# Performance work log

Measured on AMD Instinct MI355X. Metric: run time of the kernel, lower is better.

The kernel has to match this reference:

```python
import jax, jax.numpy as jnp
import numpy as np

DIM = 192
HEADS = 8
B, H, W = 8, 128, 128

def _dwconv3x3(x, w):
    # x: [B,C,H,W], w: [C,1,3,3] depthwise
    return jax.lax.conv_general_dilated(
        x, w, window_strides=(1, 1), padding=((1, 1), (1, 1)),
        dimension_numbers=('NCHW', 'OIHW', 'NCHW'),
        feature_group_count=x.shape[1])

def _proj(x, pw, dw):
    # 1x1 pointwise (as einsum) followed by 3x3 depthwise
    y = jnp.einsum('bchw,oc->bohw', x, pw)
    return _dwconv3x3(y, dw)

def setup_inputs() -> dict:
    key = jax.random.key(0)
    ks = jax.random.split(key, 9)
    s_pw = 1.0 / np.sqrt(DIM)
    s_dw = 1.0 / 3.0
    return {
        'x_feat': jax.random.normal(ks[0], (B, DIM, H, W), jnp.float32),
        'y_feat': jax.random.normal(ks[1], (B, DIM, H, W), jnp.float32),
        'q_pw': jax.random.normal(ks[2], (DIM, DIM), jnp.float32) * s_pw,
        'q_dw': jax.random.normal(ks[3], (DIM, 1, 3, 3), jnp.float32) * s_dw,
        'k_pw': jax.random.normal(ks[4], (DIM, DIM), jnp.float32) * s_pw,
        'k_dw': jax.random.normal(ks[5], (DIM, 1, 3, 3), jnp.float32) * s_dw,
        'v_pw': jax.random.normal(ks[6], (DIM, DIM), jnp.float32) * s_pw,
        'v_dw': jax.random.normal(ks[7], (DIM, 1, 3, 3), jnp.float32) * s_dw,
        'proj_w': jax.random.normal(ks[8], (DIM, DIM), jnp.float32) * s_pw,
        'temperature': jnp.ones((HEADS, 1, 1), jnp.float32),
    }

def reference(x_feat, y_feat, q_pw, q_dw, k_pw, k_dw, v_pw, v_dw, proj_w, temperature):
    b, c, h, w = x_feat.shape
    ch = c // HEADS  # channels per head
    q = _proj(x_feat, q_pw, q_dw)
    k = _proj(y_feat, k_pw, k_dw)
    v = _proj(y_feat, v_pw, v_dw)
    # b (head c) h w -> b head c (h w)
    to_heads = lambda t: t.reshape(b, HEADS, ch, h * w)
    q, k, v = to_heads(q), to_heads(k), to_heads(v)
    # L2-normalize along token dim (torch F.normalize eps=1e-12)
    q = q / jnp.maximum(jnp.linalg.norm(q, axis=-1, keepdims=True), 1e-12)
    k = k / jnp.maximum(jnp.linalg.norm(k, axis=-1, keepdims=True), 1e-12)
    attn = jnp.einsum('bhcn,bhdn->bhcd', q, k) * temperature  # [b,heads,ch,ch]
    attn = jax.nn.softmax(attn, axis=-1)
    out = jnp.einsum('bhcd,bhdn->bhcn', attn, v)
    out = out.reshape(b, c, h, w)
    out = jnp.einsum('bchw,oc->bohw', out, proj_w)
    return out
```

## Files before the change

kernel.cpp:

```cpp
#include <hip/hip_runtime.h>
#include <hip/hip_bf16.h>

#define BATCH 8
#define CDIM 192
#define HEADS 8
#define CH 24
#define HH 128
#define WW 128
#define NPIX (HH*WW)
#define NELEM (BATCH*CDIM*NPIX)
#define NP4 (NPIX/4)

#define DSLAB 16
#define NJOBS 624

typedef __attribute__((ext_vector_type(8))) short bf16x8;
typedef __attribute__((ext_vector_type(4))) float f32x4;
typedef __attribute__((ext_vector_type(4))) unsigned int u32x4;
typedef __attribute__((ext_vector_type(4))) unsigned short u16x4;

#define UNIT 100663296ull
__device__ __align__(256) unsigned char g_pool[4 * UNIT + (16u << 20)];

#define OFF_T0   (0 * UNIT)
#define OFF_QB   (1 * UNIT)
#define OFF_KB   (2 * UNIT)
#define OFF_V    (3 * UNIT)
#define OFF_MISC (4 * UNIT)
#define OFF_PART (OFF_MISC)
#define OFF_S    (OFF_MISC + 2555904ull)
#define OFF_M    (OFF_S + 159744ull)
#define OFF_MF   (OFF_M + 1179648ull)

__device__ inline unsigned short bf_rne(float x) {
  unsigned u = __float_as_uint(x);
  unsigned r = (u + 0x7fffu + ((u >> 16) & 1u)) >> 16;
  return (unsigned short)r;
}
__device__ inline void f32_split(float x, unsigned short& h, unsigned short& l) {
  h = bf_rne(x);
  float hf = __uint_as_float(((unsigned)h) << 16);
  l = bf_rne(x - hf);
}

__global__ __launch_bounds__(64) void w_to_frag(const float* __restrict__ W,
                                                unsigned short* __restrict__ F,
                                                int nb) {
  const int b = blockIdx.x / 12, mf = blockIdx.x % 12;
  const int lane = threadIdx.x;
  const int row = mf * 16 + (lane & 15);
  const size_t lo = (size_t)nb * CDIM * CDIM;
#pragma unroll
  for (int ks = 0; ks < 6; ++ks) {
    const int k0 = ks * 32 + (lane >> 4) * 8;
    const float* src = W + ((size_t)b * CDIM + row) * CDIM + k0;
    bf16x8 hv, lv;
#pragma unroll
    for (int j = 0; j < 8; ++j) {
      unsigned short h, l;
      f32_split(src[j], h, l);
      hv[j] = (short)h;
      lv[j] = (short)l;
    }
    const size_t didx = (((size_t)(blockIdx.x) * 6 + ks) * 64 + lane) * 8;
    *(bf16x8*)(F + didx) = hv;
    *(bf16x8*)(F + lo + didx) = lv;
  }
}

__global__ __launch_bounds__(256, 2) void mfma_gemm192(
    const float* __restrict__ X,
    const unsigned short* __restrict__ WF, size_t w_lo,
    int w_bstride,
    float* __restrict__ Out) {
  const int bn = blockIdx.x;
  const int b = blockIdx.y;
  const int t = threadIdx.x;
  const int lane = t & 63, wid = t >> 6;
  const int wm = wid >> 1, wn = wid & 1;
  const int kq = lane >> 4;

  __shared__ float Xs[32][132];

  const size_t wbase = (size_t)b * w_bstride;
  const float* Xb = X + (size_t)b * CDIM * NPIX;
  const int col4 = (t & 31) * 4;
  const int r0 = t >> 5;
  const int pxl = wn * 64 + (lane & 15);

  f32x4 acc[6][4];
#pragma unroll
  for (int mi = 0; mi < 6; ++mi)
#pragma unroll
    for (int ni = 0; ni < 4; ++ni) acc[mi][ni] = (f32x4){0.f, 0.f, 0.f, 0.f};

  for (int ks = 0; ks < 6; ++ks) {
    float4 st[4];
#pragma unroll
    for (int p = 0; p < 4; ++p)
      st[p] = *(const float4*)(Xb + (size_t)(ks * 32 + r0 + 8 * p) * NPIX +
                               bn * 128 + col4);
#pragma unroll
    for (int p = 0; p < 4; ++p)
      *(float4*)&Xs[r0 + 8 * p][col4 ^ ((p & 1) << 4)] = st[p];
    __syncthreads();

    bf16x8 Ah[6], Al[6];
#pragma unroll
    for (int mi = 0; mi < 6; ++mi) {
      const int mf = wm * 6 + mi;
      const size_t idx = wbase + (((size_t)(mf * 6 + ks)) * 64 + lane) * 8;
      Ah[mi] = *(const bf16x8*)(WF + idx);
      Al[mi] = *(const bf16x8*)(WF + w_lo + idx);
    }

    u32x4 Bh[4], Bl[4];
#pragma unroll
    for (int ni = 0; ni < 4; ++ni) {
      const int pxs = (pxl + ni * 16) ^ ((kq & 1) << 4);
#pragma unroll
      for (int jp = 0; jp < 4; ++jp) {
        const float x0 = Xs[kq * 8 + 2 * jp][pxs];
        const float x1 = Xs[kq * 8 + 2 * jp + 1][pxs];
        const unsigned u0 = __float_as_uint(x0);
        const unsigned u1 = __float_as_uint(x1);
        Bh[ni][jp] = (u1 & 0xffff0000u) | (u0 >> 16);
        const float rr0 = x0 - __uint_as_float(u0 & 0xffff0000u);
        const float rr1 = x1 - __uint_as_float(u1 & 0xffff0000u);
        Bl[ni][jp] = ((unsigned)bf_rne(rr1) << 16) | (unsigned)bf_rne(rr0);
      }
    }
    __syncthreads();

#pragma unroll
    for (int mi = 0; mi < 6; ++mi)
#pragma unroll
      for (int ni = 0; ni < 4; ++ni) {
        const bf16x8 bh = __builtin_bit_cast(bf16x8, Bh[ni]);
        const bf16x8 bl = __builtin_bit_cast(bf16x8, Bl[ni]);
        acc[mi][ni] = __builtin_amdgcn_mfma_f32_16x16x32_bf16(
            Ah[mi], bh, acc[mi][ni], 0, 0, 0);
        acc[mi][ni] = __builtin_amdgcn_mfma_f32_16x16x32_bf16(
            Ah[mi], bl, acc[mi][ni], 0, 0, 0);
        acc[mi][ni] = __builtin_amdgcn_mfma_f32_16x16x32_bf16(
            Al[mi], bh, acc[mi][ni], 0, 0, 0);
      }
  }

  const int ocol = bn * 128 + wn * 64 + (lane & 15);
  const int orow = wm * 96 + (lane >> 4) * 4;
#pragma unroll
  for (int mi = 0; mi < 6; ++mi)
#pragma unroll
    for (int r = 0; r < 4; ++r) {
      const int och = orow + mi * 16 + r;
      float* dst = Out + ((size_t)b * CDIM + och) * NPIX + ocol;
#pragma unroll
      for (int ni = 0; ni < 4; ++ni) dst[ni * 16] = acc[mi][ni][r];
    }
}

__global__ __launch_bounds__(256) void dwconv(const float* __restrict__ In,
                                              const float* __restrict__ Wd,
                                              float* __restrict__ Out) {
  const int idx = blockIdx.x * 256 + threadIdx.x;
  if (idx >= NELEM / 4) return;
  const int x4 = (idx & 31) * 4;
  const int y = (idx >> 5) & 127;
  const int c = (idx >> 12) % CDIM;
  const int b = idx / (32 * 128 * CDIM);

  const float* base = In + (size_t)(b * CDIM + c) * NPIX;
  float w[9];
#pragma unroll
  for (int i = 0; i < 9; ++i) w[i] = Wd[c * 9 + i];

  float acc0 = 0.f, acc1 = 0.f, acc2 = 0.f, acc3 = 0.f;
#pragma unroll
  for (int dy = 0; dy < 3; ++dy) {
    const int yy = y + dy - 1;
    if (yy < 0 || yy > 127) continue;
    const float* row = base + yy * WW;
    float vb0 = (x4 > 0) ? row[x4 - 1] : 0.f;
    const float4 m = *(const float4*)(row + x4);
    const float vb5 = (x4 + 4 < WW) ? row[x4 + 4] : 0.f;
    const float w0 = w[dy * 3 + 0], w1 = w[dy * 3 + 1], w2 = w[dy * 3 + 2];
    acc0 += w0 * vb0 + w1 * m.x + w2 * m.y;
    acc1 += w0 * m.x + w1 * m.y + w2 * m.z;
    acc2 += w0 * m.y + w1 * m.z + w2 * m.w;
    acc3 += w0 * m.z + w1 * m.w + w2 * vb5;
  }
  float4 o;
  o.x = acc0; o.y = acc1; o.z = acc2; o.w = acc3;
  *(float4*)(Out + (size_t)idx * 4) = o;
}

__global__ __launch_bounds__(256) void dwconv_bf(const float* __restrict__ In,
                                                 const float* __restrict__ Wd,
                                                 unsigned short* __restrict__ Out) {
  const int idx = blockIdx.x * 256 + threadIdx.x;
  if (idx >= NELEM / 4) return;
  const int x4 = (idx & 31) * 4;
  const int y = (idx >> 5) & 127;
  const int c = (idx >> 12) % CDIM;
  const int b = idx / (32 * 128 * CDIM);

  const float* base = In + (size_t)(b * CDIM + c) * NPIX;
  float w[9];
#pragma unroll
  for (int i = 0; i < 9; ++i) w[i] = Wd[c * 9 + i];

  float a[4] = {0.f, 0.f, 0.f, 0.f};
#pragma unroll
  for (int dy = 0; dy < 3; ++dy) {
    const int yy = y + dy - 1;
    if (yy < 0 || yy > 127) continue;
    const float* row = base + yy * WW;
    float vb0 = (x4 > 0) ? row[x4 - 1] : 0.f;
    const float4 m = *(const float4*)(row + x4);
    const float vb5 = (x4 + 4 < WW) ? row[x4 + 4] : 0.f;
    const float w0 = w[dy * 3 + 0], w1 = w[dy * 3 + 1], w2 = w[dy * 3 + 2];
    a[0] += w0 * vb0 + w1 * m.x + w2 * m.y;
    a[1] += w0 * m.x + w1 * m.y + w2 * m.z;
    a[2] += w0 * m.y + w1 * m.z + w2 * m.w;
    a[3] += w0 * m.z + w1 * m.w + w2 * vb5;
  }
  u16x4 hv, lv;
#pragma unroll
  for (int j = 0; j < 4; ++j) {
    unsigned short h, l;
    f32_split(a[j], h, l);
    hv[j] = h;
    lv[j] = l;
  }
  *(u16x4*)(Out + (size_t)idx * 4) = hv;
  *(u16x4*)(Out + NELEM + (size_t)idx * 4) = lv;
}

__global__ __launch_bounds__(256) void dots_mfma(
    const unsigned short* __restrict__ QF,
    const unsigned short* __restrict__ KF,
    float* __restrict__ Part) {
  const int bh = blockIdx.x;
  const int slab = blockIdx.y;
  const int b = bh >> 3, h = bh & 7;
  const int t = threadIdx.x;
  const int lane = t & 63, wid = t >> 6;

  const size_t rowbase = (size_t)(b * CDIM + h * CH);
  const int px0 = slab * 1024 + wid * 256;
  const int rr = lane & 15;
  const int j8 = (lane >> 4) * 8;

  f32x4 accx[2][2], aqq[2], aqhl[2], akk[2], akhl[2];
#pragma unroll
  for (int mi = 0; mi < 2; ++mi) {
#pragma unroll
    for (int ni = 0; ni < 2; ++ni) accx[mi][ni] = (f32x4){0.f, 0.f, 0.f, 0.f};
    aqq[mi] = (f32x4){0.f, 0.f, 0.f, 0.f};
    aqhl[mi] = (f32x4){0.f, 0.f, 0.f, 0.f};
    akk[mi] = (f32x4){0.f, 0.f, 0.f, 0.f};
    akhl[mi] = (f32x4){0.f, 0.f, 0.f, 0.f};
  }

  auto load_step = [&](int s, bf16x8 (&qh)[2], bf16x8 (&ql)[2],
                       bf16x8 (&kh)[2], bf16x8 (&kl)[2]) {
    const int px = px0 + s * 32 + j8;
#pragma unroll
    for (int mi = 0; mi < 2; ++mi) {
      const size_t off = (rowbase + mi * 16 + rr) * (size_t)NPIX + px;
      qh[mi] = *(const bf16x8*)(QF + off);
      ql[mi] = *(const bf16x8*)(QF + NELEM + off);
      kh[mi] = *(const bf16x8*)(KF + off);
      kl[mi] = *(const bf16x8*)(KF + NELEM + off);
    }
  };
  auto mfma_step = [&](bf16x8 (&qh)[2], bf16x8 (&ql)[2], bf16x8 (&kh)[2],
                       bf16x8 (&kl)[2]) {
#pragma unroll
    for (int mi = 0; mi < 2; ++mi) {
#pragma unroll
      for (int ni = 0; ni < 2; ++ni) {
        accx[mi][ni] = __builtin_amdgcn_mfma_f32_16x16x32_bf16(
            qh[mi], kh[ni], accx[mi][ni], 0, 0, 0);
        accx[mi][ni] = __builtin_amdgcn_mfma_f32_16x16x32_bf16(
            qh[mi], kl[ni], accx[mi][ni], 0, 0, 0);
        accx[mi][ni] = __builtin_amdgcn_mfma_f32_16x16x32_bf16(
            ql[mi], kh[ni], accx[mi][ni], 0, 0, 0);
      }
      aqq[mi] = __builtin_amdgcn_mfma_f32_16x16x32_bf16(qh[mi], qh[mi],
                                                        aqq[mi], 0, 0, 0);
      aqhl[mi] = __builtin_amdgcn_mfma_f32_16x16x32_bf16(qh[mi], ql[mi],
                                                         aqhl[mi], 0, 0, 0);
      akk[mi] = __builtin_amdgcn_mfma_f32_16x16x32_bf16(kh[mi], kh[mi],
                                                        akk[mi], 0, 0, 0);
      akhl[mi] = __builtin_amdgcn_mfma_f32_16x16x32_bf16(kh[mi], kl[mi],
                                                         akhl[mi], 0, 0, 0);
    }
  };

  bf16x8 Aqh[2], Aql[2], Akh[2], Akl[2];
  bf16x8 Bqh[2], Bql[2], Bkh[2], Bkl[2];
  load_step(0, Aqh, Aql, Akh, Akl);
#pragma unroll
  for (int s = 0; s < 8; s += 2) {
    if (s + 1 < 8) load_step(s + 1, Bqh, Bql, Bkh, Bkl);
    mfma_step(Aqh, Aql, Akh, Akl);
    if (s + 2 < 8) load_step(s + 2, Aqh, Aql, Akh, Akl);
    mfma_step(Bqh, Bql, Bkh, Bkl);
  }

  __shared__ float xls[4][24][24];
  __shared__ float qls[4][24], kls[4][24];
  const int col = lane & 15;
  const int rbase = (lane >> 4) * 4;
#pragma unroll
  for (int mi = 0; mi < 2; ++mi) {
#pragma unroll
    for (int ni = 0; ni < 2; ++ni) {
      const int d = ni * 16 + col;
      if (d < 24) {
#pragma unroll
        for (int r = 0; r < 4; ++r) {
          const int c = mi * 16 + rbase + r;
          if (c < 24) xls[wid][c][d] = accx[mi][ni][r];
        }
      }
    }
    const int cc = mi * 16 + col;
    const int rd = col - rbase;
    if (cc < 24 && rd >= 0 && rd < 4) {
      qls[wid][cc] = aqq[mi][rd] + 2.f * aqhl[mi][rd];
      kls[wid][cc] = akk[mi][rd] + 2.f * akhl[mi][rd];
    }
  }
  __syncthreads();

  float* P = Part + ((size_t)bh * DSLAB + slab) * NJOBS;
  for (int j = t; j < 576; j += 256) {
    const int c = j / 24, d = j % 24;
    P[j] = xls[0][c][d] + xls[1][c][d] + xls[2][c][d] + xls[3][c][d];
  }
  if (t < 24) P[576 + t] = qls[0][t] + qls[1][t] + qls[2][t] + qls[3][t];
  else if (t >= 32 && t < 56) {
    const int c = t - 32;
    P[600 + c] = kls[0][c] + kls[1][c] + kls[2][c] + kls[3][c];
  }
}

__global__ __launch_bounds__(640) void dots_reduce(const float* __restrict__ Part,
                                                   float* __restrict__ S) {
  const int bh = blockIdx.x;
  const int job = threadIdx.x;
  if (job >= NJOBS) return;
  float s = 0.f;
  for (int i = 0; i < DSLAB; ++i)
    s += Part[((size_t)bh * DSLAB + i) * NJOBS + job];
  S[bh * NJOBS + job] = s;
}

__global__ __launch_bounds__(576) void build_M(const float* __restrict__ S,
                                               const float* __restrict__ PW,
                                               const float* __restrict__ Temp,
                                               float* __restrict__ M) {
  const int b = blockIdx.x, h = blockIdx.y;
  const int bh = b * 8 + h;
  __shared__ float att[CH][CH];
  __shared__ float qn[CH], kn[CH];
  const int t = threadIdx.x;
  const float* Sb = S + (size_t)bh * NJOBS;

  if (t < CH) {
    qn[t] = fmaxf(sqrtf(Sb[576 + t]), 1e-12f);
    kn[t] = fmaxf(sqrtf(Sb[600 + t]), 1e-12f);
  }
  __syncthreads();
  const float temp = Temp[h];
  if (t < 576) {
    const int c = t / 24, d = t % 24;
    att[c][d] = Sb[t] / (qn[c] * kn[d]) * temp;
  }
  __syncthreads();
  if (t < CH) {
    float mx = -1e30f;
    for (int d = 0; d < CH; ++d) mx = fmaxf(mx, att[t][d]);
    float sum = 0.f;
    for (int d = 0; d < CH; ++d) {
      const float e = __expf(att[t][d] - mx);
      att[t][d] = e;
      sum += e;
    }
    const float inv = 1.f / sum;
    for (int d = 0; d < CH; ++d) att[t][d] *= inv;
  }
  __syncthreads();
  for (int i = t; i < CDIM * CH; i += 576) {
    const int o = i / CH, d = i % CH;
    float s = 0.f;
#pragma unroll
    for (int c = 0; c < CH; ++c) s += PW[o * CDIM + h * CH + c] * att[c][d];
    M[((size_t)b * CDIM + o) * CDIM + h * CH + d] = s;
  }
}


extern "C" void kernel_launch(void* const* d_in, const int* in_sizes, int n_in,
                              void* d_out, int out_size, void* d_ws, size_t ws_size,
                              hipStream_t stream) {
  const float* x_feat = (const float*)d_in[0];
  const float* y_feat = (const float*)d_in[1];
  const float* q_pw   = (const float*)d_in[2];
  const float* q_dw   = (const float*)d_in[3];
  const float* k_pw   = (const float*)d_in[4];
  const float* k_dw   = (const float*)d_in[5];
  const float* v_pw   = (const float*)d_in[6];
  const float* v_dw   = (const float*)d_in[7];
  const float* proj_w = (const float*)d_in[8];
  const float* temp   = (const float*)d_in[9];
  float* out = (float*)d_out;

  unsigned char* pool;
  (void)hipGetSymbolAddress((void**)&pool, HIP_SYMBOL(g_pool));
  float* t0 = (float*)(pool + OFF_T0);
  unsigned short* QB = (unsigned short*)(pool + OFF_QB);
  unsigned short* KB = (unsigned short*)(pool + OFF_KB);
  float* v  = (float*)(pool + OFF_V);
  float* part = (float*)(pool + OFF_PART);
  float* S    = (float*)(pool + OFF_S);
  float* M    = (float*)(pool + OFF_M);
  unsigned short* MF = (unsigned short*)(pool + OFF_MF);

  unsigned short* WQF = MF + 2ull * 8 * CDIM * CDIM;
  unsigned short* WKF = WQF + 2ull * CDIM * CDIM;
  unsigned short* WVF = WKF + 2ull * CDIM * CDIM;

  const size_t w1_lo = (size_t)1 * CDIM * CDIM;
  const size_t w8_lo = (size_t)8 * CDIM * CDIM;

  const dim3 ggrid(NPIX / 128, BATCH);
  const int dwgrid = (NELEM / 4) / 256;

  w_to_frag<<<12, 64, 0, stream>>>(q_pw, WQF, 1);
  w_to_frag<<<12, 64, 0, stream>>>(k_pw, WKF, 1);
  w_to_frag<<<12, 64, 0, stream>>>(v_pw, WVF, 1);

  mfma_gemm192<<<ggrid, 256, 0, stream>>>(x_feat, WQF, w1_lo, 0, t0);
  dwconv_bf<<<dwgrid, 256, 0, stream>>>(t0, q_dw, QB);
  mfma_gemm192<<<ggrid, 256, 0, stream>>>(y_feat, WKF, w1_lo, 0, t0);
  dwconv_bf<<<dwgrid, 256, 0, stream>>>(t0, k_dw, KB);

  dots_mfma<<<dim3(64, DSLAB), 256, 0, stream>>>(QB, KB, part);
  dots_reduce<<<64, 640, 0, stream>>>(part, S);
  build_M<<<dim3(BATCH, HEADS), 576, 0, stream>>>(S, proj_w, temp, M);
  w_to_frag<<<8 * 12, 64, 0, stream>>>(M, MF, 8);

  mfma_gemm192<<<ggrid, 256, 0, stream>>>(y_feat, WVF, w1_lo, 0, t0);
  dwconv<<<dwgrid, 256, 0, stream>>>(t0, v_dw, v);

  mfma_gemm192<<<ggrid, 256, 0, stream>>>(v, MF, w8_lo, CDIM * CDIM, out);
}
```

Before: 444.5 us.

## Double-buffer pre-split bf16 LDS tiles in pointwise GEMM with 512 threads

The pointwise GEMM now splits fp32 activations into bf16 hi/lo once, when staging into a double-buffered LDS tile stored k-contiguous, so each wave reads ready-made bf16x8 fragments with vector LDS loads. The global load for the next k-slice is issued before the MFMAs on the current one, which removes one barrier per iteration and overlaps load latency with compute. The block grows to 8 waves (2x4) with half the per-wave accumulator tile, raising occupancy and lowering register pressure. The cost is scalar 16-bit transposed LDS writes, which may cause bank conflicts, and weight fragments are now reloaded per mi inside the loop.

```diff
diff --git a/kernel.cpp b/kernel.cpp
--- a/kernel.cpp
+++ b/kernel.cpp
@@ -16,7 +16,6 @@
 
 typedef __attribute__((ext_vector_type(8))) short bf16x8;
 typedef __attribute__((ext_vector_type(4))) float f32x4;
-typedef __attribute__((ext_vector_type(4))) unsigned int u32x4;
 typedef __attribute__((ext_vector_type(4))) unsigned short u16x4;
 
 #define UNIT 100663296ull
@@ -68,7 +67,9 @@
   }
 }
 
-__global__ __launch_bounds__(256, 2) void mfma_gemm192(
+#define BSTR 40
+
+__global__ __launch_bounds__(512, 2) void mfma_gemm192(
     const float* __restrict__ X,
     const unsigned short* __restrict__ WF, size_t w_lo,
     int w_bstride,
@@ -77,77 +78,98 @@
   const int b = blockIdx.y;
   const int t = threadIdx.x;
   const int lane = t & 63, wid = t >> 6;
-  const int wm = wid >> 1, wn = wid & 1;
-  const int kq = lane >> 4;
-
-  __shared__ float Xs[32][132];
+  const int wm = wid >> 2;
+  const int wn = wid & 3;
+
+  __shared__ unsigned short Bs[2][2][128 * BSTR];
 
   const size_t wbase = (size_t)b * w_bstride;
   const float* Xb = X + (size_t)b * CDIM * NPIX;
-  const int col4 = (t & 31) * 4;
-  const int r0 = t >> 5;
-  const int pxl = wn * 64 + (lane & 15);
-
-  f32x4 acc[6][4];
+
+  const int sr = t >> 4;
+  const int sp = (t & 15) * 8;
+
+  auto stage_write = [&](int buf, float4 v0, float4 v1) {
+    unsigned short* H = &Bs[buf][0][0];
+    unsigned short* L = &Bs[buf][1][0];
+    const float* p0 = (const float*)&v0;
+    const float* p1 = (const float*)&v1;
+#pragma unroll
+    for (int i = 0; i < 4; ++i) {
+      unsigned short h, l;
+      f32_split(p0[i], h, l);
+      H[(sp + i) * BSTR + sr] = h;
+      L[(sp + i) * BSTR + sr] = l;
+    }
+#pragma unroll
+    for (int i = 0; i < 4; ++i) {
+      unsigned short h, l;
+      f32_split(p1[i], h, l);
+      H[(sp + 4 + i) * BSTR + sr] = h;
+      L[(sp + 4 + i) * BSTR + sr] = l;
+    }
+  };
+
+  const int pxl = wn * 32 + (lane & 15);
+  const int k0 = (lane >> 4) * 8;
+
+  f32x4 acc[6][2];
 #pragma unroll
   for (int mi = 0; mi < 6; ++mi)
 #pragma unroll
-    for (int ni = 0; ni < 4; ++ni) acc[mi][ni] = (f32x4){0.f, 0.f, 0.f, 0.f};
-
+    for (int ni = 0; ni < 2; ++ni) acc[mi][ni] = (f32x4){0.f, 0.f, 0.f, 0.f};
+
+  {
+    const float4 v0 = *(const float4*)(Xb + (size_t)sr * NPIX + bn * 128 + sp);
+    const float4 v1 =
+        *(const float4*)(Xb + (size_t)sr * NPIX + bn * 128 + sp + 4);
+    stage_write(0, v0, v1);
+  }
+  __syncthreads();
+
+  int cur = 0;
   for (int ks = 0; ks < 6; ++ks) {
-    float4 st[4];
-#pragma unroll
-    for (int p = 0; p < 4; ++p)
-      st[p] = *(const float4*)(Xb + (size_t)(ks * 32 + r0 + 8 * p) * NPIX +
-                               bn * 128 + col4);
-#pragma unroll
-    for (int p = 0; p < 4; ++p)
-      *(float4*)&Xs[r0 + 8 * p][col4 ^ ((p & 1) << 4)] = st[p];
-    __syncthreads();
-
-    bf16x8 Ah[6], Al[6];
+    float4 n0, n1;
+    if (ks < 5) {
+      n0 = *(const float4*)(Xb + (size_t)((ks + 1) * 32 + sr) * NPIX +
+                            bn * 128 + sp);
+      n1 = *(const float4*)(Xb + (size_t)((ks + 1) * 32 + sr) * NPIX +
+                            bn * 128 + sp + 4);
+    }
+
+    bf16x8 Bh[2], Bl[2];
+#pragma unroll
+    for (int ni = 0; ni < 2; ++ni) {
+      const int addr = (pxl + ni * 16) * BSTR + k0;
+      Bh[ni] = *(const bf16x8*)&Bs[cur][0][addr];
+      Bl[ni] = *(const bf16x8*)&Bs[cur][1][addr];
+    }
+
 #pragma unroll
     for (int mi = 0; mi < 6; ++mi) {
       const int mf = wm * 6 + mi;
       const size_t idx = wbase + (((size_t)(mf * 6 + ks)) * 64 + lane) * 8;
-      Ah[mi] = *(const bf16x8*)(WF + idx);
-      Al[mi] = *(const bf16x8*)(WF + w_lo + idx);
-    }
-
-    u32x4 Bh[4], Bl[4];
-#pragma unroll
-    for (int ni = 0; ni < 4; ++ni) {
-      const int pxs = (pxl + ni * 16) ^ ((kq & 1) << 4);
-#pragma unroll
-      for (int jp = 0; jp < 4; ++jp) {
-        const float x0 = Xs[kq * 8 + 2 * jp][pxs];
-        const float x1 = Xs[kq * 8 + 2 * jp + 1][pxs];
-        const unsigned u0 = __float_as_uint(x0);
-        const unsigned u1 = __float_as_uint(x1);
-        Bh[ni][jp] = (u1 & 0xffff0000u) | (u0 >> 16);
-        const float rr0 = x0 - __uint_as_float(u0 & 0xffff0000u);
-        const float rr1 = x1 - __uint_as_float(u1 & 0xffff0000u);
-        Bl[ni][jp] = ((unsigned)bf_rne(rr1) << 16) | (unsigned)bf_rne(rr0);
+      const bf16x8 Ah = *(const bf16x8*)(WF + idx);
+      const bf16x8 Al = *(const bf16x8*)(WF + w_lo + idx);
+#pragma unroll
+      for (int ni = 0; ni < 2; ++ni) {
+        acc[mi][ni] = __builtin_amdgcn_mfma_f32_16x16x32_bf16(
+            Ah, Bh[ni], acc[mi][ni], 0, 0, 0);
+        acc[mi][ni] = __builtin_amdgcn_mfma_f32_16x16x32_bf16(
+            Ah, Bl[ni], acc[mi][ni], 0, 0, 0);
+        acc[mi][ni] = __builtin_amdgcn_mfma_f32_16x16x32_bf16(
+            Al, Bh[ni], acc[mi][ni], 0, 0, 0);
       }
     }
-    __syncthreads();
-
-#pragma unroll
-    for (int mi = 0; mi < 6; ++mi)
-#pragma unroll
-      for (int ni = 0; ni < 4; ++ni) {
-        const bf16x8 bh = __builtin_bit_cast(bf16x8, Bh[ni]);
-        const bf16x8 bl = __builtin_bit_cast(bf16x8, Bl[ni]);
-        acc[mi][ni] = __builtin_amdgcn_mfma_f32_16x16x32_bf16(
-            Ah[mi], bh, acc[mi][ni], 0, 0, 0);
-        acc[mi][ni] = __builtin_amdgcn_mfma_f32_16x16x32_bf16(
-            Ah[mi], bl, acc[mi][ni], 0, 0, 0);
-        acc[mi][ni] = __builtin_amdgcn_mfma_f32_16x16x32_bf16(
-            Al[mi], bh, acc[mi][ni], 0, 0, 0);
-      }
-  }
-
-  const int ocol = bn * 128 + wn * 64 + (lane & 15);
+
+    if (ks < 5) {
+      stage_write(cur ^ 1, n0, n1);
+      __syncthreads();
+      cur ^= 1;
+    }
+  }
+
+  const int ocol = bn * 128 + wn * 32 + (lane & 15);
   const int orow = wm * 96 + (lane >> 4) * 4;
 #pragma unroll
   for (int mi = 0; mi < 6; ++mi)
@@ -155,8 +177,8 @@
     for (int r = 0; r < 4; ++r) {
       const int och = orow + mi * 16 + r;
       float* dst = Out + ((size_t)b * CDIM + och) * NPIX + ocol;
-#pragma unroll
-      for (int ni = 0; ni < 4; ++ni) dst[ni * 16] = acc[mi][ni][r];
+      dst[0] = acc[mi][0][r];
+      dst[16] = acc[mi][1][r];
     }
 }
 
@@ -444,9 +466,9 @@
   w_to_frag<<<12, 64, 0, stream>>>(k_pw, WKF, 1);
   w_to_frag<<<12, 64, 0, stream>>>(v_pw, WVF, 1);
 
-  mfma_gemm192<<<ggrid, 256, 0, stream>>>(x_feat, WQF, w1_lo, 0, t0);
+  mfma_gemm192<<<ggrid, 512, 0, stream>>>(x_feat, WQF, w1_lo, 0, t0);
   dwconv_bf<<<dwgrid, 256, 0, stream>>>(t0, q_dw, QB);
-  mfma_gemm192<<<ggrid, 256, 0, stream>>>(y_feat, WKF, w1_lo, 0, t0);
+  mfma_gemm192<<<ggrid, 512, 0, stream>>>(y_feat, WKF, w1_lo, 0, t0);
   dwconv_bf<<<dwgrid, 256, 0, stream>>>(t0, k_dw, KB);
 
   dots_mfma<<<dim3(64, DSLAB), 256, 0, stream>>>(QB, KB, part);
@@ -454,8 +476,8 @@
   build_M<<<dim3(BATCH, HEADS), 576, 0, stream>>>(S, proj_w, temp, M);
   w_to_frag<<<8 * 12, 64, 0, stream>>>(M, MF, 8);
 
-  mfma_gemm192<<<ggrid, 256, 0, stream>>>(y_feat, WVF, w1_lo, 0, t0);
+  mfma_gemm192<<<ggrid, 512, 0, stream>>>(y_feat, WVF, w1_lo, 0, t0);
   dwconv<<<dwgrid, 256, 0, stream>>>(t0, v_dw, v);
 
-  mfma_gemm192<<<ggrid, 256, 0, stream>>>(v, MF, w8_lo, CDIM * CDIM, out);
-}
+  mfma_gemm192<<<ggrid, 512, 0, stream>>>(v, MF, w8_lo, CDIM * CDIM, out);
+}
```

Result: slower. 550.8 us (+23.9%).
